# Kernel optimization log

Hardware: AMD Instinct MI355X
Metric: run time of the kernel (lower is better)

## Reference

```python
import jax, jax.numpy as jnp
import numpy as np


def _lyndon_indices(c, d):
    """All Lyndon words of length <= d over alphabet {0..c-1} via Duval's algorithm,
    mapped to flat indices into the flattened signature (levels 1..d concatenated,
    first letter most significant within each level). Static numpy computation."""
    words = []
    w = [-1]
    while w:
        w[-1] += 1
        words.append(tuple(w))
        m = len(w)
        while len(w) < d:
            w.append(w[len(w) - m])
        while w and w[-1] == c - 1:
            w.pop()
    words.sort(key=lambda t: (len(t), t))  # group by word length, lexicographic within
    offsets = np.concatenate([[0], np.cumsum([c ** k for k in range(1, d + 1)])])
    idx = []
    for word in words:
        pos = 0
        for letter in word:
            pos = pos * c + letter
        idx.append(int(offsets[len(word) - 1]) + pos)
    return np.asarray(idx, dtype=np.int64)


def _split_levels(sig, c, d):
    levels, start = [], 0
    for k in range(1, d + 1):
        n = c ** k
        levels.append(sig[:, start:start + n])  # (B, c^k)
        start += n
    return levels


def _mul_by_S(P, S, d):
    """Graded product P (x) S in the truncated tensor algebra (zero scalar parts).
    P[i], S[i] are level-(i+1) components of shape (B, c^(i+1)) or None."""
    B = S[0].shape[0]
    out = [None] * d
    for m in range(d):  # output level m+1
        acc = None
        for i in range(m):  # P level i+1 combines with S level m-i
            if P[i] is None:
                continue
            t = jnp.einsum('bi,bj->bij', P[i], S[m - 1 - i]).reshape(B, -1)
            acc = t if acc is None else acc + t
        out[m] = acc
    return out


def _log_signature_flat(sig, c, d):
    """log(1 + S) truncated at depth d, flattened levels 1..d."""
    S = _split_levels(sig, c, d)
    L = list(S)  # n=1 term (coefficient +1)
    P = S
    for n in range(2, d + 1):
        P = _mul_by_S(P, S, d)  # P = S^{(x) n}, levels < n are None
        coef = ((-1.0) ** (n + 1)) / n
        for k in range(d):
            if P[k] is not None:
                L[k] = L[k] + coef * P[k]
    return jnp.concatenate(L, axis=1)


def setup_inputs() -> dict:
    key = jax.random.key(0)
    channels, depth, batch = 8, 6, 64
    width = sum(channels ** k for k in range(1, depth + 1))  # 299592
    signature = jax.random.normal(key, (batch, width), dtype=jnp.float32) * 0.1
    return {"signature": signature, "channels": channels, "depth": depth}


def reference(signature, channels, depth):
    idx = jnp.asarray(_lyndon_indices(channels, depth))
    log_sig = _log_signature_flat(signature, channels, depth)  # (B, width)
    return log_sig[:, idx]  # Lyndon-word coefficients ('words' mode)
```

## Files before the change

### kernel.cpp

```cpp
#include <hip/hip_runtime.h>

#define NWIDTH 299592
#define NOUT   51360

typedef unsigned long long ull;
typedef unsigned short u16;

__device__ const int g_B2[8] = {8, 15, 21, 26, 30, 33, 35, 36};
__device__ const int g_B3[8] = {36, 92, 134, 164, 184, 196, 202, 204};
__device__ const int g_B4[8] = {204, 624, 897, 1062, 1152, 1194, 1209, 1212};
__device__ const int g_B5[8] = {1212, 4404, 6210, 7140, 7560, 7716, 7758, 7764};
__device__ const int g_C6[8] = {0, 24052, 35861, 41016, 42926, 43480, 43587, 43596};
__device__ const int g_dj1[9] = {0, 0, 0, 0, 0, 1, 1, 2, 3};
__device__ const int g_dr0[9] = {0, 4811, 9622, 14432, 19242, 24052, 29957, 35861, 41016};
__device__ const int g_dr1[9] = {4811, 9622, 14432, 19242, 24052, 29957, 35861, 41016, 42926};

__device__ __forceinline__ bool is_lyndon6(unsigned p) {
  const unsigned mask = (1u << 18) - 1u;
#pragma unroll
  for (int k = 1; k < 6; ++k) {
    unsigned rot = ((p << (3 * k)) & mask) | (p >> (18 - 3 * k));
    if (p >= rot) return false;
  }
  return true;
}
__device__ __forceinline__ bool is_lyndon(unsigned p, int n) {
  const unsigned nb = 3u * (unsigned)n;
  const unsigned mask = (1u << nb) - 1u;
  for (int k = 1; k < n; ++k) {
    unsigned rot = ((p << (3 * k)) & mask) | (p >> (nb - 3 * k));
    if (p >= rot) return false;
  }
  return true;
}

__global__ __launch_bounds__(1024) void lyndon_prep(u16* __restrict__ pos16) {
  __shared__ int wsum[16];
  const int tid = threadIdx.x, lane = tid & 63, wv = tid >> 6;
  const int j = blockIdx.x;
  const unsigned pb = ((unsigned)j << 15) | ((unsigned)tid << 5);
  unsigned lm = 0;
  int c = 0;
  for (int i = 0; i < 32; ++i)
    if (is_lyndon6(pb | (unsigned)i)) { lm |= 1u << i; ++c; }
  int pref = c;
  for (int d = 1; d < 64; d <<= 1) { int t = __shfl_up(pref, d); if (lane >= d) pref += t; }
  if (lane == 63) wsum[wv] = pref;
  __syncthreads();
  int base = 0;
  for (int i = 0; i < wv; ++i) base += wsum[i];
  int ex = g_C6[j] + base + pref - c;
  unsigned m = lm;
  const int p0 = tid << 5;
  while (m) {
    const int bit = __builtin_ctz(m);
    pos16[ex++] = (u16)(p0 + bit);
    m &= m - 1;
  }
}

#define L_S3  0
#define L_S2  512
#define L_S1  576
#define L_PA  584
#define L_PB  1168
#define L_A2  1752
#define L_A3  1760
#define L_A4  1824
#define L_W4  2336
#define L_W5  2344
#define L_A5  2352
#define L_PL  6448
#define L_TOT 9404

__global__ __launch_bounds__(512)
void logsig_fused(const float* __restrict__ sig,
                  const u16* __restrict__ pos16,
                  float* __restrict__ out) {
  __shared__ __align__(16) float sm[L_TOT];
  int* W4i = (int*)(sm + L_W4);
  int* W5i = (int*)(sm + L_W5);
  u16* PL  = (u16*)(sm + L_PL);

  const int tid = threadIdx.x, lane = tid & 63, wv = tid >> 6;
  const int bid = blockIdx.x;
  const int xcd = bid & 7;
  const int rr  = bid >> 3;
  const int b   = xcd * 8 + (rr >> 4);
  const int u   = rr & 15;
  const bool isalg = (u < 7);
  const int j1 = isalg ? u : g_dj1[u - 7];
  int r0, r1;
  if (isalg) {
    r0 = (j1 >= 4) ? g_C6[j1] : 0;
    r1 = (j1 >= 4) ? g_C6[j1 + 1] : 0;
  } else {
    r0 = g_dr0[u - 7];
    r1 = g_dr1[u - 7];
  }
  const int cnt = r1 - r0;

  const float* __restrict__ S   = sig + (size_t)b * NWIDTH;
  const float* __restrict__ S4g = S + 584;
  const float* __restrict__ S5g = S + 4680;
  const float* __restrict__ S6j = S + 37448 + (size_t)j1 * 32768;
  float* __restrict__ outb = out + (size_t)b * NOUT;

  const float p1 = S[j1];
  const float c2p1 = -0.5f * p1;
  const int q4 = tid << 2;

  sm[L_S3 + tid] = S[72 + tid];
  if (tid < 64) sm[L_S2 + tid] = S[8 + tid];
  if (tid < 8)  sm[L_S1 + tid] = S[tid];
  if (tid < 8)  sm[L_PA + tid]      = S[8 + j1 * 8 + tid];
  if (tid < 64) sm[L_PA + 8 + tid]  = S[72 + j1 * 64 + tid];
  sm[L_PA + 72 + tid] = S4g[j1 * 512 + tid];
  for (int i = tid; i < cnt; i += 512) PL[i] = pos16[r0 + i];
  float p5[8];
  {
    float4 va = *(const float4*)(S5g + j1 * 4096 + q4);
    float4 vb = *(const float4*)(S5g + j1 * 4096 + 2048 + q4);
    p5[0] = va.x; p5[1] = va.y; p5[2] = va.z; p5[3] = va.w;
    p5[4] = vb.x; p5[5] = vb.y; p5[6] = vb.z; p5[7] = vb.w;
  }
  float a5[8] = {0.f, 0.f, 0.f, 0.f, 0.f, 0.f, 0.f, 0.f};
  float a4 = 0.f, a3 = 0.f, a2 = 0.f;

  ull m4 = 0;
  unsigned fm5a = 0, fm5b = 0;
  int exA = 0, exB = 0;
  if (isalg) {
    bool f4 = is_lyndon(((unsigned)j1 << 9) | (unsigned)tid, 4);
    m4 = __ballot(f4);
    if (lane == 0) W4i[wv] = __popcll(m4);
    int c5a = 0, c5b = 0;
#pragma unroll
    for (int e = 0; e < 4; ++e) {
      if (is_lyndon(((unsigned)j1 << 12) | (unsigned)(q4 + e), 5)) { fm5a |= 1u << e; ++c5a; }
      if (is_lyndon(((unsigned)j1 << 12) | (unsigned)(2048 + q4 + e), 5)) { fm5b |= 1u << e; ++c5b; }
    }
    int prefpk = c5a | (c5b << 16);
    for (int d = 1; d < 64; d <<= 1) { int t = __shfl_up(prefpk, d); if (lane >= d) prefpk += t; }
    if (lane == 63) W5i[wv] = prefpk;
    exA = (prefpk & 0xffff) - c5a;
    exB = (prefpk >> 16) - c5b;
  }
  __syncthreads();

  const float s1t = sm[L_S1 + (tid & 7)];
  float s1q4[4];
#pragma unroll
  for (int e = 0; e < 4; ++e) s1q4[e] = sm[L_S1 + ((tid & 1) << 2) + e];

  const float coefs[7] = {0.f, 0.f, -0.5f, 1.f / 3.f, -0.25f, 0.2f, -1.f / 6.f};
#pragma unroll
  for (int n = 2; n <= 5; ++n) {
    const float coef = coefs[n];
    const int RP = (n & 1) ? L_PB : L_PA;
    const int WP = (n & 1) ? L_PA : L_PB;
    a4 += coef * sm[RP + 72 + tid];
    if (tid < 64) a3 += coef * sm[RP + 8 + tid];
    if (tid < 8)  a2 += coef * sm[RP + tid];
    float t4 = sm[RP + 8 + (tid >> 3)] * s1t
             + sm[RP + (tid >> 6)] * sm[L_S2 + (tid & 63)];
    if (n == 2) t4 += p1 * sm[L_S3 + tid];
    float t3 = 0.f, t2 = 0.f;
    if (tid < 64) {
      t3 = sm[RP + (tid >> 3)] * s1t;
      if (n == 2) t3 += p1 * sm[L_S2 + tid];
    }
    if (tid < 8 && n == 2) t2 = p1 * s1t;
    {
      const float rp4a = sm[RP + 72 + (tid >> 1)];
      const float rp4b = sm[RP + 72 + 256 + (tid >> 1)];
      const float rp3a = sm[RP + 8 + (tid >> 4)];
      const float rp3b = sm[RP + 8 + 32 + (tid >> 4)];
      const float rp2a = sm[RP + (tid >> 7)];
      const float rp2b = sm[RP + 4 + (tid >> 7)];
      const float4 s2v = *(const float4*)(sm + L_S2 + (q4 & 63));
      const float4 s3v = *(const float4*)(sm + L_S3 + (q4 & 511));
      const float s2q[4] = {s2v.x, s2v.y, s2v.z, s2v.w};
      const float s3q[4] = {s3v.x, s3v.y, s3v.z, s3v.w};
#pragma unroll
      for (int e = 0; e < 4; ++e) {
        a5[e]     += coef * p5[e];
        a5[4 + e] += coef * p5[4 + e];
        p5[e]     = rp4a * s1q4[e] + rp3a * s2q[e] + rp2a * s3q[e];
        p5[4 + e] = rp4b * s1q4[e] + rp3b * s2q[e] + rp2b * s3q[e];
      }
      if (n == 2) {
        const float4 s4va = *(const float4*)(S4g + q4);
        const float4 s4vb = *(const float4*)(S4g + 2048 + q4);
        const float s4qa[4] = {s4va.x, s4va.y, s4va.z, s4va.w};
        const float s4qb[4] = {s4vb.x, s4vb.y, s4vb.z, s4vb.w};
#pragma unroll
        for (int e = 0; e < 4; ++e) {
          p5[e] += p1 * s4qa[e];
          p5[4 + e] += p1 * s4qb[e];
        }
      }
    }
    sm[WP + 72 + tid] = t4;
    if (tid < 64) sm[WP + 8 + tid] = t3;
    if (tid < 8)  sm[WP + tid]     = t2;
    __syncthreads();
  }
#pragma unroll
  for (int e = 0; e < 8; ++e) a5[e] += coefs[6] * p5[e];

  sm[L_A4 + tid] = a4;
  if (tid < 64) sm[L_A3 + tid] = a3;
  if (tid < 8)  sm[L_A2 + tid] = a2;
  *(float4*)(sm + L_A5 + q4)        = make_float4(a5[0], a5[1], a5[2], a5[3]);
  *(float4*)(sm + L_A5 + 2048 + q4) = make_float4(a5[4], a5[5], a5[6], a5[7]);
  __syncthreads();

  if (isalg) {
    float l2v = 0.f, l3v = 0.f;
    if (tid < 8)
      l2v = sm[L_S2 + j1 * 8 + tid] + c2p1 * s1t;
    if (tid < 64)
      l3v = sm[L_S3 + j1 * 64 + tid] + sm[L_A2 + (tid >> 3)] * s1t
          + c2p1 * sm[L_S2 + tid];
    const float l4v = S4g[j1 * 512 + tid] + sm[L_A3 + (tid >> 3)] * s1t
                    + sm[L_A2 + (tid >> 6)] * sm[L_S2 + (tid & 63)]
                    + c2p1 * sm[L_S3 + tid];
    float l5a[4], l5b[4];
    {
      const float4 via  = *(const float4*)(S5g + j1 * 4096 + q4);
      const float4 vib  = *(const float4*)(S5g + j1 * 4096 + 2048 + q4);
      const float4 s4va = *(const float4*)(S4g + q4);
      const float4 s4vb = *(const float4*)(S4g + 2048 + q4);
      const float4 s2v  = *(const float4*)(sm + L_S2 + (q4 & 63));
      const float4 s3v  = *(const float4*)(sm + L_S3 + (q4 & 511));
      const float l5ia[4] = {via.x, via.y, via.z, via.w};
      const float l5ib[4] = {vib.x, vib.y, vib.z, vib.w};
      const float s4qa[4] = {s4va.x, s4va.y, s4va.z, s4va.w};
      const float s4qb[4] = {s4vb.x, s4vb.y, s4vb.z, s4vb.w};
      const float s2q[4]  = {s2v.x, s2v.y, s2v.z, s2v.w};
      const float s3q[4]  = {s3v.x, s3v.y, s3v.z, s3v.w};
      const float a4a = sm[L_A4 + (tid >> 1)],  a4b = sm[L_A4 + 256 + (tid >> 1)];
      const float a3a = sm[L_A3 + (tid >> 4)],  a3b = sm[L_A3 + 32 + (tid >> 4)];
      const float a2a = sm[L_A2 + (tid >> 7)],  a2b = sm[L_A2 + 4 + (tid >> 7)];
#pragma unroll
      for (int e = 0; e < 4; ++e) {
        l5a[e] = l5ia[e] + a4a * s1q4[e] + a3a * s2q[e] + a2a * s3q[e] + c2p1 * s4qa[e];
        l5b[e] = l5ib[e] + a4b * s1q4[e] + a3b * s2q[e] + a2b * s3q[e] + c2p1 * s4qb[e];
      }
    }
    if (tid == 0) {
      outb[j1] = p1;
      if (j1 == 0) outb[7] = sm[L_S1 + 7];
    }
    if (tid < 8 && tid > j1) outb[g_B2[j1] + tid - j1 - 1] = l2v;
    if (tid < 64) {
      bool f3 = is_lyndon(((unsigned)j1 << 6) | (unsigned)tid, 3);
      ull m3 = __ballot(f3);
      if (f3) outb[g_B3[j1] + __popcll(m3 & ((1ull << lane) - 1ull))] = l3v;
    }
    {
      int base = 0;
      for (int i = 0; i < wv; ++i) base += W4i[i];
      if ((m4 >> lane) & 1ull)
        outb[g_B4[j1] + base + __popcll(m4 & ((1ull << lane) - 1ull))] = l4v;
    }
    {
      int baseA = 0, baseB = 0, totalA = 0;
#pragma unroll
      for (int i = 0; i < 8; ++i) {
        int w = W5i[i];
        totalA += w & 0xffff;
        if (i < wv) { baseA += w & 0xffff; baseB += w >> 16; }
      }
      int slotA = g_B5[j1] + baseA + exA;
      int slotB = g_B5[j1] + totalA + baseB + exB;
#pragma unroll
      for (int e = 0; e < 4; ++e)
        if ((fm5a >> e) & 1u) outb[slotA++] = l5a[e];
#pragma unroll
      for (int e = 0; e < 4; ++e)
        if ((fm5b >> e) & 1u) outb[slotB++] = l5b[e];
    }
  }

  for (int i = tid; i < cnt; i += 512) {
    const int pl = PL[i];
    float v = S6j[pl]
            + sm[L_A5 + (pl >> 3)] * sm[L_S1 + (pl & 7)]
            + sm[L_A4 + (pl >> 6)] * sm[L_S2 + (pl & 63)]
            + sm[L_A3 + (pl >> 9)] * sm[L_S3 + (pl & 511)]
            + sm[L_A2 + (pl >> 12)] * S4g[pl & 4095]
            + c2p1 * S5g[pl];
    outb[7764 + r0 + i] = v;
  }
}


extern "C" void kernel_launch(void* const* d_in, const int* in_sizes, int n_in,
                              void* d_out, int out_size, void* d_ws, size_t ws_size,
                              hipStream_t stream) {
  const float* sig = (const float*)d_in[0];
  float* out = (float*)d_out;
  u16* pos16 = (u16*)d_ws;

  lyndon_prep<<<7, 1024, 0, stream>>>(pos16);
  logsig_fused<<<1024, 512, 0, stream>>>(sig, pos16, out);
}
```

Baseline: 41.56 us.

## Rebalance level-6 work across 16 per-batch blocks and unroll gather loop by two

```diff
diff --git a/kernel.cpp b/kernel.cpp
--- a/kernel.cpp
+++ b/kernel.cpp
@@ -11,9 +11,14 @@
 __device__ const int g_B4[8] = {204, 624, 897, 1062, 1152, 1194, 1209, 1212};
 __device__ const int g_B5[8] = {1212, 4404, 6210, 7140, 7560, 7716, 7758, 7764};
 __device__ const int g_C6[8] = {0, 24052, 35861, 41016, 42926, 43480, 43587, 43596};
-__device__ const int g_dj1[9] = {0, 0, 0, 0, 0, 1, 1, 2, 3};
-__device__ const int g_dr0[9] = {0, 4811, 9622, 14432, 19242, 24052, 29957, 35861, 41016};
-__device__ const int g_dr1[9] = {4811, 9622, 14432, 19242, 24052, 29957, 35861, 41016, 42926};
+__device__ const int g_uj1[16] = {0,0,0,0,0,0, 1,1,1,1, 2,2, 3, 4, 5, 6};
+__device__ const int g_ur0[16] = {0, 4009, 8018, 12027, 16036, 20044,
+                                  24052, 27005, 29957, 32909,
+                                  35861, 38439, 41016, 42926, 43480, 43587};
+__device__ const int g_ur1[16] = {4009, 8018, 12027, 16036, 20044, 24052,
+                                  27005, 29957, 32909, 35861,
+                                  38439, 41016, 42926, 43480, 43587, 43596};
+__device__ const int g_ualg[16] = {1,0,0,0,0,0, 1,0,0,0, 1,0, 1, 1, 1, 1};
 
 __device__ __forceinline__ bool is_lyndon6(unsigned p) {
   const unsigned mask = (1u << 18) - 1u;
@@ -71,7 +76,7 @@
 #define L_W5  2344
 #define L_A5  2352
 #define L_PL  6448
-#define L_TOT 9404
+#define L_TOT 8456
 
 __global__ __launch_bounds__(512)
 void logsig_fused(const float* __restrict__ sig,
@@ -88,16 +93,9 @@
   const int rr  = bid >> 3;
   const int b   = xcd * 8 + (rr >> 4);
   const int u   = rr & 15;
-  const bool isalg = (u < 7);
-  const int j1 = isalg ? u : g_dj1[u - 7];
-  int r0, r1;
-  if (isalg) {
-    r0 = (j1 >= 4) ? g_C6[j1] : 0;
-    r1 = (j1 >= 4) ? g_C6[j1 + 1] : 0;
-  } else {
-    r0 = g_dr0[u - 7];
-    r1 = g_dr1[u - 7];
-  }
+  const int j1  = g_uj1[u];
+  const bool isalg = g_ualg[u] != 0;
+  const int r0 = g_ur0[u], r1 = g_ur1[u];
   const int cnt = r1 - r0;
 
   const float* __restrict__ S   = sig + (size_t)b * NWIDTH;
@@ -284,7 +282,30 @@
     }
   }
 
-  for (int i = tid; i < cnt; i += 512) {
+  float* __restrict__ outr = outb + 7764 + r0;
+  int i = tid;
+  for (; i + 512 < cnt; i += 1024) {
+    const int pl0 = PL[i];
+    const int pl1 = PL[i + 512];
+    const float x60 = S6j[pl0], x61 = S6j[pl1];
+    const float x50 = S5g[pl0], x51 = S5g[pl1];
+    const float x40 = S4g[pl0 & 4095], x41 = S4g[pl1 & 4095];
+    float v0 = x60
+             + sm[L_A5 + (pl0 >> 3)] * sm[L_S1 + (pl0 & 7)]
+             + sm[L_A4 + (pl0 >> 6)] * sm[L_S2 + (pl0 & 63)]
+             + sm[L_A3 + (pl0 >> 9)] * sm[L_S3 + (pl0 & 511)]
+             + sm[L_A2 + (pl0 >> 12)] * x40
+             + c2p1 * x50;
+    float v1 = x61
+             + sm[L_A5 + (pl1 >> 3)] * sm[L_S1 + (pl1 & 7)]
+             + sm[L_A4 + (pl1 >> 6)] * sm[L_S2 + (pl1 & 63)]
+             + sm[L_A3 + (pl1 >> 9)] * sm[L_S3 + (pl1 & 511)]
+             + sm[L_A2 + (pl1 >> 12)] * x41
+             + c2p1 * x51;
+    outr[i] = v0;
+    outr[i + 512] = v1;
+  }
+  if (i < cnt) {
     const int pl = PL[i];
     float v = S6j[pl]
             + sm[L_A5 + (pl >> 3)] * sm[L_S1 + (pl & 7)]
@@ -292,7 +313,7 @@
             + sm[L_A3 + (pl >> 9)] * sm[L_S3 + (pl & 511)]
             + sm[L_A2 + (pl >> 12)] * S4g[pl & 4095]
             + c2p1 * S5g[pl];
-    outb[7764 + r0 + i] = v;
+    outr[i] = v;
   }
 }
 
```

Result: slower. 43.86 us (+5.5%).

## Split fused log-signature kernel into algebra and level-6 evaluation kernels

Applied to the files above, without the earlier changes.

```diff
diff --git a/kernel.cpp b/kernel.cpp
--- a/kernel.cpp
+++ b/kernel.cpp
@@ -11,9 +11,6 @@
 __device__ const int g_B4[8] = {204, 624, 897, 1062, 1152, 1194, 1209, 1212};
 __device__ const int g_B5[8] = {1212, 4404, 6210, 7140, 7560, 7716, 7758, 7764};
 __device__ const int g_C6[8] = {0, 24052, 35861, 41016, 42926, 43480, 43587, 43596};
-__device__ const int g_dj1[9] = {0, 0, 0, 0, 0, 1, 1, 2, 3};
-__device__ const int g_dr0[9] = {0, 4811, 9622, 14432, 19242, 24052, 29957, 35861, 41016};
-__device__ const int g_dr1[9] = {4811, 9622, 14432, 19242, 24052, 29957, 35861, 41016, 42926};
 
 __device__ __forceinline__ bool is_lyndon6(unsigned p) {
   const unsigned mask = (1u << 18) - 1u;
@@ -70,35 +67,23 @@
 #define L_W4  2336
 #define L_W5  2344
 #define L_A5  2352
-#define L_PL  6448
-#define L_TOT 9404
+#define L_TOT 6448
 
 __global__ __launch_bounds__(512)
-void logsig_fused(const float* __restrict__ sig,
-                  const u16* __restrict__ pos16,
-                  float* __restrict__ out) {
+void logsig_algebra(const float* __restrict__ sig,
+                    const u16* __restrict__ pos16,
+                    float* __restrict__ Aws,
+                    float* __restrict__ out) {
   __shared__ __align__(16) float sm[L_TOT];
   int* W4i = (int*)(sm + L_W4);
   int* W5i = (int*)(sm + L_W5);
-  u16* PL  = (u16*)(sm + L_PL);
 
   const int tid = threadIdx.x, lane = tid & 63, wv = tid >> 6;
   const int bid = blockIdx.x;
   const int xcd = bid & 7;
-  const int rr  = bid >> 3;
-  const int b   = xcd * 8 + (rr >> 4);
-  const int u   = rr & 15;
-  const bool isalg = (u < 7);
-  const int j1 = isalg ? u : g_dj1[u - 7];
-  int r0, r1;
-  if (isalg) {
-    r0 = (j1 >= 4) ? g_C6[j1] : 0;
-    r1 = (j1 >= 4) ? g_C6[j1 + 1] : 0;
-  } else {
-    r0 = g_dr0[u - 7];
-    r1 = g_dr1[u - 7];
-  }
-  const int cnt = r1 - r0;
+  const int g   = bid >> 3;
+  const int b   = xcd * 8 + g / 7;
+  const int j1  = g % 7;
 
   const float* __restrict__ S   = sig + (size_t)b * NWIDTH;
   const float* __restrict__ S4g = S + 584;
@@ -116,7 +101,6 @@
   if (tid < 8)  sm[L_PA + tid]      = S[8 + j1 * 8 + tid];
   if (tid < 64) sm[L_PA + 8 + tid]  = S[72 + j1 * 64 + tid];
   sm[L_PA + 72 + tid] = S4g[j1 * 512 + tid];
-  for (int i = tid; i < cnt; i += 512) PL[i] = pos16[r0 + i];
   float p5[8];
   {
     float4 va = *(const float4*)(S5g + j1 * 4096 + q4);
@@ -130,7 +114,7 @@
   ull m4 = 0;
   unsigned fm5a = 0, fm5b = 0;
   int exA = 0, exB = 0;
-  if (isalg) {
+  {
     bool f4 = is_lyndon(((unsigned)j1 << 9) | (unsigned)tid, 4);
     m4 = __ballot(f4);
     if (lane == 0) W4i[wv] = __popcll(m4);
@@ -214,85 +198,126 @@
   if (tid < 8)  sm[L_A2 + tid] = a2;
   *(float4*)(sm + L_A5 + q4)        = make_float4(a5[0], a5[1], a5[2], a5[3]);
   *(float4*)(sm + L_A5 + 2048 + q4) = make_float4(a5[4], a5[5], a5[6], a5[7]);
+  if (j1 < 4) {
+    float* Aw = Aws + (size_t)((b << 2) + j1) * 4680;
+    if (tid < 8)  Aw[tid] = a2;
+    if (tid < 64) Aw[8 + tid] = a3;
+    Aw[72 + tid] = a4;
+    *(float4*)(Aw + 584 + q4)        = make_float4(a5[0], a5[1], a5[2], a5[3]);
+    *(float4*)(Aw + 584 + 2048 + q4) = make_float4(a5[4], a5[5], a5[6], a5[7]);
+  }
   __syncthreads();
 
-  if (isalg) {
-    float l2v = 0.f, l3v = 0.f;
-    if (tid < 8)
-      l2v = sm[L_S2 + j1 * 8 + tid] + c2p1 * s1t;
-    if (tid < 64)
-      l3v = sm[L_S3 + j1 * 64 + tid] + sm[L_A2 + (tid >> 3)] * s1t
-          + c2p1 * sm[L_S2 + tid];
-    const float l4v = S4g[j1 * 512 + tid] + sm[L_A3 + (tid >> 3)] * s1t
-                    + sm[L_A2 + (tid >> 6)] * sm[L_S2 + (tid & 63)]
-                    + c2p1 * sm[L_S3 + tid];
-    float l5a[4], l5b[4];
-    {
-      const float4 via  = *(const float4*)(S5g + j1 * 4096 + q4);
-      const float4 vib  = *(const float4*)(S5g + j1 * 4096 + 2048 + q4);
-      const float4 s4va = *(const float4*)(S4g + q4);
-      const float4 s4vb = *(const float4*)(S4g + 2048 + q4);
-      const float4 s2v  = *(const float4*)(sm + L_S2 + (q4 & 63));
-      const float4 s3v  = *(const float4*)(sm + L_S3 + (q4 & 511));
-      const float l5ia[4] = {via.x, via.y, via.z, via.w};
-      const float l5ib[4] = {vib.x, vib.y, vib.z, vib.w};
-      const float s4qa[4] = {s4va.x, s4va.y, s4va.z, s4va.w};
-      const float s4qb[4] = {s4vb.x, s4vb.y, s4vb.z, s4vb.w};
-      const float s2q[4]  = {s2v.x, s2v.y, s2v.z, s2v.w};
-      const float s3q[4]  = {s3v.x, s3v.y, s3v.z, s3v.w};
-      const float a4a = sm[L_A4 + (tid >> 1)],  a4b = sm[L_A4 + 256 + (tid >> 1)];
-      const float a3a = sm[L_A3 + (tid >> 4)],  a3b = sm[L_A3 + 32 + (tid >> 4)];
-      const float a2a = sm[L_A2 + (tid >> 7)],  a2b = sm[L_A2 + 4 + (tid >> 7)];
-#pragma unroll
-      for (int e = 0; e < 4; ++e) {
-        l5a[e] = l5ia[e] + a4a * s1q4[e] + a3a * s2q[e] + a2a * s3q[e] + c2p1 * s4qa[e];
-        l5b[e] = l5ib[e] + a4b * s1q4[e] + a3b * s2q[e] + a2b * s3q[e] + c2p1 * s4qb[e];
-      }
-    }
-    if (tid == 0) {
-      outb[j1] = p1;
-      if (j1 == 0) outb[7] = sm[L_S1 + 7];
-    }
-    if (tid < 8 && tid > j1) outb[g_B2[j1] + tid - j1 - 1] = l2v;
-    if (tid < 64) {
-      bool f3 = is_lyndon(((unsigned)j1 << 6) | (unsigned)tid, 3);
-      ull m3 = __ballot(f3);
-      if (f3) outb[g_B3[j1] + __popcll(m3 & ((1ull << lane) - 1ull))] = l3v;
-    }
-    {
-      int base = 0;
-      for (int i = 0; i < wv; ++i) base += W4i[i];
-      if ((m4 >> lane) & 1ull)
-        outb[g_B4[j1] + base + __popcll(m4 & ((1ull << lane) - 1ull))] = l4v;
-    }
-    {
-      int baseA = 0, baseB = 0, totalA = 0;
-#pragma unroll
-      for (int i = 0; i < 8; ++i) {
-        int w = W5i[i];
-        totalA += w & 0xffff;
-        if (i < wv) { baseA += w & 0xffff; baseB += w >> 16; }
-      }
-      int slotA = g_B5[j1] + baseA + exA;
-      int slotB = g_B5[j1] + totalA + baseB + exB;
-#pragma unroll
-      for (int e = 0; e < 4; ++e)
-        if ((fm5a >> e) & 1u) outb[slotA++] = l5a[e];
-#pragma unroll
-      for (int e = 0; e < 4; ++e)
-        if ((fm5b >> e) & 1u) outb[slotB++] = l5b[e];
-    }
-  }
-
-  for (int i = tid; i < cnt; i += 512) {
-    const int pl = PL[i];
+  float l2v = 0.f, l3v = 0.f;
+  if (tid < 8)
+    l2v = sm[L_S2 + j1 * 8 + tid] + c2p1 * s1t;
+  if (tid < 64)
+    l3v = sm[L_S3 + j1 * 64 + tid] + sm[L_A2 + (tid >> 3)] * s1t
+        + c2p1 * sm[L_S2 + tid];
+  const float l4v = S4g[j1 * 512 + tid] + sm[L_A3 + (tid >> 3)] * s1t
+                  + sm[L_A2 + (tid >> 6)] * sm[L_S2 + (tid & 63)]
+                  + c2p1 * sm[L_S3 + tid];
+  float l5a[4], l5b[4];
+  {
+    const float4 via  = *(const float4*)(S5g + j1 * 4096 + q4);
+    const float4 vib  = *(const float4*)(S5g + j1 * 4096 + 2048 + q4);
+    const float4 s4va = *(const float4*)(S4g + q4);
+    const float4 s4vb = *(const float4*)(S4g + 2048 + q4);
+    const float4 s2v  = *(const float4*)(sm + L_S2 + (q4 & 63));
+    const float4 s3v  = *(const float4*)(sm + L_S3 + (q4 & 511));
+    const float l5ia[4] = {via.x, via.y, via.z, via.w};
+    const float l5ib[4] = {vib.x, vib.y, vib.z, vib.w};
+    const float s4qa[4] = {s4va.x, s4va.y, s4va.z, s4va.w};
+    const float s4qb[4] = {s4vb.x, s4vb.y, s4vb.z, s4vb.w};
+    const float s2q[4]  = {s2v.x, s2v.y, s2v.z, s2v.w};
+    const float s3q[4]  = {s3v.x, s3v.y, s3v.z, s3v.w};
+    const float a4a = sm[L_A4 + (tid >> 1)],  a4b = sm[L_A4 + 256 + (tid >> 1)];
+    const float a3a = sm[L_A3 + (tid >> 4)],  a3b = sm[L_A3 + 32 + (tid >> 4)];
+    const float a2a = sm[L_A2 + (tid >> 7)],  a2b = sm[L_A2 + 4 + (tid >> 7)];
+#pragma unroll
+    for (int e = 0; e < 4; ++e) {
+      l5a[e] = l5ia[e] + a4a * s1q4[e] + a3a * s2q[e] + a2a * s3q[e] + c2p1 * s4qa[e];
+      l5b[e] = l5ib[e] + a4b * s1q4[e] + a3b * s2q[e] + a2b * s3q[e] + c2p1 * s4qb[e];
+    }
+  }
+  if (tid == 0) {
+    outb[j1] = p1;
+    if (j1 == 0) outb[7] = sm[L_S1 + 7];
+  }
+  if (tid < 8 && tid > j1) outb[g_B2[j1] + tid - j1 - 1] = l2v;
+  if (tid < 64) {
+    bool f3 = is_lyndon(((unsigned)j1 << 6) | (unsigned)tid, 3);
+    ull m3 = __ballot(f3);
+    if (f3) outb[g_B3[j1] + __popcll(m3 & ((1ull << lane) - 1ull))] = l3v;
+  }
+  {
+    int base = 0;
+    for (int i = 0; i < wv; ++i) base += W4i[i];
+    if ((m4 >> lane) & 1ull)
+      outb[g_B4[j1] + base + __popcll(m4 & ((1ull << lane) - 1ull))] = l4v;
+  }
+  {
+    int baseA = 0, baseB = 0, totalA = 0;
+#pragma unroll
+    for (int i = 0; i < 8; ++i) {
+      int w = W5i[i];
+      totalA += w & 0xffff;
+      if (i < wv) { baseA += w & 0xffff; baseB += w >> 16; }
+    }
+    int slotA = g_B5[j1] + baseA + exA;
+    int slotB = g_B5[j1] + totalA + baseB + exB;
+#pragma unroll
+    for (int e = 0; e < 4; ++e)
+      if ((fm5a >> e) & 1u) outb[slotA++] = l5a[e];
+#pragma unroll
+    for (int e = 0; e < 4; ++e)
+      if ((fm5b >> e) & 1u) outb[slotB++] = l5b[e];
+  }
+
+  if (j1 >= 4) {
+    const int r0 = g_C6[j1];
+    const int cnt = g_C6[j1 + 1] - r0;
+    for (int i = tid; i < cnt; i += 512) {
+      const int pl = pos16[r0 + i];
+      float v = S6j[pl]
+              + sm[L_A5 + (pl >> 3)] * sm[L_S1 + (pl & 7)]
+              + sm[L_A4 + (pl >> 6)] * sm[L_S2 + (pl & 63)]
+              + sm[L_A3 + (pl >> 9)] * sm[L_S3 + (pl & 511)]
+              + sm[L_A2 + (pl >> 12)] * S4g[pl & 4095]
+              + c2p1 * S5g[pl];
+      outb[7764 + r0 + i] = v;
+    }
+  }
+}
+
+__global__ __launch_bounds__(256)
+void logsig_eval6(const float* __restrict__ sig,
+                  const float* __restrict__ Aws,
+                  const u16* __restrict__ pos16,
+                  float* __restrict__ out) {
+  const int bid = blockIdx.x;
+  const int xcd = bid & 7;
+  const int g   = bid >> 3;
+  const int b   = xcd * 8 + (g >> 5);
+  const int chunk = g & 31;
+  const int r0 = chunk * 1342;
+  const int r1 = (r0 + 1342 < 42926) ? r0 + 1342 : 42926;
+
+  const float* __restrict__ S = sig + (size_t)b * NWIDTH;
+  float* __restrict__ outr = out + (size_t)b * NOUT + 7764;
+
+  for (int r = r0 + threadIdx.x; r < r1; r += 256) {
+    const int pl = pos16[r];
+    const int j1 = (r >= 24052) + (r >= 35861) + (r >= 41016);
+    const float* __restrict__ Aw = Aws + (size_t)((b << 2) + j1) * 4680;
+    const float* __restrict__ S6j = S + 37448 + (j1 << 15);
     float v = S6j[pl]
-            + sm[L_A5 + (pl >> 3)] * sm[L_S1 + (pl & 7)]
-            + sm[L_A4 + (pl >> 6)] * sm[L_S2 + (pl & 63)]
-            + sm[L_A3 + (pl >> 9)] * sm[L_S3 + (pl & 511)]
-            + sm[L_A2 + (pl >> 12)] * S4g[pl & 4095]
-            + c2p1 * S5g[pl];
-    outb[7764 + r0 + i] = v;
+            + Aw[584 + (pl >> 3)] * S[pl & 7]
+            + Aw[72 + (pl >> 6)] * S[8 + (pl & 63)]
+            + Aw[8 + (pl >> 9)] * S[72 + (pl & 511)]
+            + Aw[pl >> 12] * S[584 + (pl & 4095)]
+            + (-0.5f * S[j1]) * S[4680 + pl];
+    outr[r] = v;
   }
 }
 
@@ -302,8 +327,10 @@
                               hipStream_t stream) {
   const float* sig = (const float*)d_in[0];
   float* out = (float*)d_out;
-  u16* pos16 = (u16*)d_ws;
+  float* Aws = (float*)d_ws;
+  u16* pos16 = (u16*)(Aws + 64 * 4 * 4680);
 
   lyndon_prep<<<7, 1024, 0, stream>>>(pos16);
-  logsig_fused<<<1024, 512, 0, stream>>>(sig, pos16, out);
-}
+  logsig_algebra<<<448, 512, 0, stream>>>(sig, pos16, Aws, out);
+  logsig_eval6<<<2048, 256, 0, stream>>>(sig, Aws, pos16, out);
+}
```

After: 45.34 us. +9.1%, slower.
